# Performance work log

Hardware: AMD Instinct MI355X
Metric: run time of the kernel (lower is better)

Reference implementation:

```python
import jax, jax.numpy as jnp
import numpy as np

E, S, L, H, C = 32, 64, 20, 512, 32  # episodes, steps, max_comm_len, hidden_size, comm_shape
STD_MIN, STD_MAX = 2.0611536e-09, 7.389056  # exp(-20), exp(2)


def setup_inputs() -> dict:
    key = jax.random.key(0)
    ks = jax.random.split(key, 12)
    def p(k, shape):
        return jax.random.normal(k, shape, jnp.float32) * 0.02
    return {
        'x': jax.random.normal(ks[0], (E, S, H), jnp.float32),
        'Wr': p(ks[1], (2 * H, H)), 'br': jnp.zeros((H,), jnp.float32),
        'Wz': p(ks[2], (2 * H, H)), 'bz': jnp.zeros((H,), jnp.float32),
        'Wn': p(ks[3], (2 * H, H)), 'bn': jnp.zeros((H,), jnp.float32),
        'conv_w1': p(ks[4], (H // 4, H, 1)), 'conv_b1': jnp.zeros((H // 4,), jnp.float32),
        'conv_w3': p(ks[5], (H // 4, H, 3)), 'conv_b3': jnp.zeros((H // 4,), jnp.float32),
        'conv_w5': p(ks[6], (H // 4, H, 5)), 'conv_b5': jnp.zeros((H // 4,), jnp.float32),
        'conv_w7': p(ks[7], (H // 4, H, 7)), 'conv_b7': jnp.zeros((H // 4,), jnp.float32),
        'prelu_a': jnp.asarray(0.25, jnp.float32),
        'W_mu': p(ks[8], (H, C)), 'b_mu': jnp.zeros((C,), jnp.float32),
        'W_std': p(ks[9], (H, C)), 'b_std': jnp.zeros((C,), jnp.float32),
        'eps': jax.random.normal(ks[10], (E, S, L, C), jnp.float32),
    }


def reference(x, Wr, br, Wz, bz, Wn, bn,
              conv_w1, conv_b1, conv_w3, conv_b3, conv_w5, conv_b5, conv_w7, conv_b7,
              prelu_a, W_mu, b_mu, W_std, b_std, eps):
    B = E * S
    xf = x.reshape(B, H)  # same input fed to the RNN at every comm step

    def step(h, _):
        xh = jnp.concatenate([xf, h], -1)
        r = jax.nn.sigmoid(xh @ Wr + br)
        z = jax.nn.sigmoid(xh @ Wz + bz)
        n = jnp.tanh(jnp.concatenate([xf, r * h], -1) @ Wn + bn)
        h_new = (1.0 - z) * n + z * h  # time_constant=1 -> h = new GRU state
        return h_new, h_new

    h0 = jnp.zeros((B, H), x.dtype)
    _, hs = jax.lax.scan(step, h0, None, length=L)  # (L, B, H)
    comm_h = jnp.transpose(hs, (1, 2, 0))  # (B, H, L) -- NCW layout for conv

    dn = ('NCH', 'OIH', 'NCH')
    def conv(w, b, k):
        pad = (k - 1) // 2
        y = jax.lax.conv_general_dilated(comm_h, w, (1,), [(pad, pad)], dimension_numbers=dn)
        return y + b[None, :, None]

    y = jnp.concatenate([
        conv(conv_w1, conv_b1, 1),
        conv(conv_w3, conv_b3, 3),
        conv(conv_w5, conv_b5, 5),
        conv(conv_w7, conv_b7, 7),
    ], axis=1)  # (B, H, L)
    y = jnp.where(y >= 0, y, prelu_a * y)  # PReLU; dropout is identity in eval
    y = jnp.transpose(y, (0, 2, 1)).reshape(E, S, L, H)

    mu = y @ W_mu + b_mu
    std = jnp.clip(jax.nn.softplus(y @ W_std + b_std), STD_MIN, STD_MAX)
    comm = mu + eps * std  # reparameterized Normal sample
    comm_out = jnp.tanh(comm)
    log2pi = jnp.asarray(np.log(2.0 * np.pi), jnp.float32)
    log_prob = (-0.5 * ((comm - mu) / std) ** 2 - jnp.log(std) - 0.5 * log2pi
                - jnp.log(1.0 - comm_out ** 2 + 1e-6))
    log_prob = jnp.mean(log_prob, -1, keepdims=True)  # (E,S,L,1)
    log_prob = jnp.mean(log_prob, -2)  # (E,S,1)
    return comm_out, log_prob
```

## Files before the change

kernel.cpp:

```cpp
#include <hip/hip_runtime.h>
#include <hip/hip_bf16.h>

typedef __hip_bfloat16 bf16;
typedef short short8 __attribute__((ext_vector_type(8)));
typedef float floatx4 __attribute__((ext_vector_type(4)));

#define BDIM 2048
#define HDIM 512
#define LDIM 20
#define CDIM 32

__device__ __forceinline__ float sigm(float x) { return 1.0f / (1.0f + expf(-x)); }

__device__ __forceinline__ void ll16(const short* g, short* l)
{
    __builtin_amdgcn_global_load_lds(
        (const __attribute__((address_space(1))) void*)g,
        (__attribute__((address_space(3))) void*)l, 16, 0, 0);
}
#define WAITVM(N) asm volatile("s_waitcnt vmcnt(" #N ")" ::: "memory")

__device__ __forceinline__ void gemm_tile_ll(
    const short* __restrict__ A, int lda,
    const short* __restrict__ Bt, int ldb,
    int K, short* lds, floatx4 (&acc)[4][4], int tid)
{
    short* As = lds;
    short* Bs = lds + 128 * 32;
    const int wave = tid >> 6, lane = tid & 63;
    const int wm = wave & 1, wn = wave >> 1;
    const int m16 = lane & 15, quad = lane >> 4;
    const int lrow = lane >> 2;
    const int lcol = (lane & 3) * 8;

    for (int k0 = 0; k0 < K; k0 += 32) {
        __syncthreads();
#pragma unroll
        for (int seg = 0; seg < 2; ++seg) {
            const int sg = wave + seg * 4;
            ll16(A  + (size_t)(sg * 16 + lrow) * lda + k0 + lcol, As + sg * 512);
            ll16(Bt + (size_t)(sg * 16 + lrow) * ldb + k0 + lcol, Bs + sg * 512);
        }
        WAITVM(0);
        __syncthreads();
        short8 af[4], bfr[4];
#pragma unroll
        for (int i = 0; i < 4; ++i)
            af[i] = *(short8*)(As + (wm * 64 + i * 16 + m16) * 32 + quad * 8);
#pragma unroll
        for (int j = 0; j < 4; ++j)
            bfr[j] = *(short8*)(Bs + (wn * 64 + j * 16 + m16) * 32 + quad * 8);
#pragma unroll
        for (int i = 0; i < 4; ++i)
#pragma unroll
            for (int j = 0; j < 4; ++j)
                acc[i][j] = __builtin_amdgcn_mfma_f32_16x16x32_bf16(
                    af[i], bfr[j], acc[i][j], 0, 0, 0);
    }
}

__global__ __launch_bounds__(256) void k_prep_all(
    const float* __restrict__ x, bf16* __restrict__ xb,
    const float* __restrict__ Wr, const float* __restrict__ Wz,
    const float* __restrict__ Wn, bf16* __restrict__ Wfrag,
    const float* __restrict__ w1, const float* __restrict__ w3,
    const float* __restrict__ w5, const float* __restrict__ w7,
    bf16* __restrict__ wt,
    const float* __restrict__ Wmu, const float* __restrict__ Wstd,
    bf16* __restrict__ Wh_t, bf16* __restrict__ Wx_t,
    unsigned* __restrict__ ctr)
{
    __shared__ float tile[32][33];
    const int bid = blockIdx.x, tid = threadIdx.x;
    if (bid < 4096) {
        int i = bid * 256 + tid;
        xb[i] = (bf16)x[i];
    } else if (bid < 7168) {
        int idx = (bid - 4096) * 256 + tid;
        int e = idx & 7, lane = (idx >> 3) & 63;
        int t2 = idx >> 9;
        int f = t2 % 6, jk = t2 / 6;
        int kc = jk & 15, j = jk >> 4;
        int ftype = f >> 1;
        int col = j * 32 + (f & 1) * 16 + (lane & 15);
        int k = kc * 32 + ((lane >> 4) << 3) + e;
        const float* W = (ftype == 0) ? Wr : (ftype == 1) ? Wz : Wn;
        Wfrag[idx] = (bf16)W[(size_t)(512 + k) * 512 + col];
    } else if (bid < 11264) {
        int idx = (bid - 7168) * 256 + tid;
        int g, base;
        if (idx < 65536)       { g = 0; base = 0;      }
        else if (idx < 262144) { g = 1; base = 65536;  }
        else if (idx < 589824) { g = 2; base = 262144; }
        else                   { g = 3; base = 589824; }
        int rel = idx - base;
        int k = 2 * g + 1;
        int ci = rel & 511;
        int t2 = rel >> 9;
        int co = t2 & 127;
        int tap = t2 >> 7;
        const float* w = (g == 0) ? w1 : (g == 1) ? w3 : (g == 2) ? w5 : w7;
        wt[idx] = (bf16)w[((size_t)co * 512 + ci) * k + tap];
    } else if (bid < 11392) {
        int idx = (bid - 11264) * 256 + tid;
        int n = idx >> 9, k = idx & 511;
        float v = (n < 32) ? Wmu[(size_t)k * 32 + n]
                           : Wstd[(size_t)k * 32 + (n - 32)];
        Wh_t[idx] = (bf16)v;
    } else if (bid < 12160) {
        int rel = bid - 11392;
        int z = rel >> 8, xy = rel & 255;
        const float* src = (z == 0) ? Wr : (z == 1) ? Wz : Wn;
        bf16* d = Wx_t + (size_t)z * 262144;
        int tx = tid & 31, ty = tid >> 5;
        int k0 = (xy & 15) * 32, n0 = (xy >> 4) * 32;
#pragma unroll
        for (int i = 0; i < 32; i += 8)
            tile[ty + i][tx] = src[(size_t)(k0 + ty + i) * 512 + n0 + tx];
        __syncthreads();
#pragma unroll
        for (int i = 0; i < 32; i += 8)
            d[(size_t)(n0 + ty + i) * 512 + k0 + tx] = (bf16)tile[tx][ty + i];
    } else {
        ((unsigned*)ctr)[tid * 2]     = 0u;
        ((unsigned*)ctr)[tid * 2 + 1] = 0u;
    }
}

__global__ __launch_bounds__(256) void k_gx(
    const bf16* __restrict__ xb, const bf16* __restrict__ Wx_t,
    const float* __restrict__ br, const float* __restrict__ bz,
    const float* __restrict__ bn, bf16* __restrict__ gxb)
{
    __shared__ short lds[2 * 128 * 32];
    const int tid = threadIdx.x;
    const int row0 = blockIdx.x * 128, col0 = blockIdx.y * 128;
    floatx4 acc[4][4];
#pragma unroll
    for (int i = 0; i < 4; ++i)
#pragma unroll
        for (int j = 0; j < 4; ++j) acc[i][j] = (floatx4)0.0f;
    gemm_tile_ll((const short*)xb + (size_t)row0 * 512, 512,
                 (const short*)Wx_t + (size_t)col0 * 512, 512, 512, lds, acc, tid);
    const int wave = tid >> 6, lane = tid & 63;
    const int wm = wave & 1, wn = wave >> 1;
    const int m16 = lane & 15, quad = lane >> 4;
#pragma unroll
    for (int i = 0; i < 4; ++i)
#pragma unroll
        for (int j = 0; j < 4; ++j)
#pragma unroll
            for (int reg = 0; reg < 4; ++reg) {
                int b = row0 + wm * 64 + i * 16 + quad * 4 + reg;
                int n = col0 + wn * 64 + j * 16 + m16;
                float bias = (n < 512) ? br[n] : (n < 1024) ? bz[n - 512] : bn[n - 1024];
                gxb[(size_t)b * 1536 + n] = (bf16)(acc[i][j][reg] + bias);
            }
}

__device__ __forceinline__ void gbar2(unsigned* flags, int j, unsigned target,
                                      bool fast, int tid)
{
    WAITVM(0);
    __syncthreads();
    if (tid < 64) {
        if (tid == 0) {
            if (!fast) __threadfence();
            __hip_atomic_store(flags + j, target, __ATOMIC_RELAXED,
                               __HIP_MEMORY_SCOPE_AGENT);
        }
        unsigned v; int guard = 0;
        do {
            v = (tid < 16) ? __hip_atomic_load(flags + tid, __ATOMIC_RELAXED,
                                               __HIP_MEMORY_SCOPE_AGENT)
                           : target;
        } while (__ballot(v >= target) != ~0ull && ++guard < (1 << 18));
        if (!fast) { if (tid == 0) __threadfence(); }
        else asm volatile("buffer_inv" ::: "memory");
    }
    __syncthreads();
}

template<int NF>
__device__ __forceinline__ void phase_reg(
    const short* __restrict__ srcw, const short* __restrict__ wl,
    int f0, int lane, floatx4 (&acc)[NF])
{
    const short* g = srcw + (size_t)(lane & 15) * 512 + (lane >> 4) * 8;
    short8 a[16];
#pragma unroll
    for (int kc = 0; kc < 16; ++kc)
        a[kc] = *(const short8*)(g + kc * 32);
#pragma unroll
    for (int kc = 0; kc < 16; ++kc) {
        short8 bfr[NF];
#pragma unroll
        for (int f = 0; f < NF; ++f)
            bfr[f] = *(short8*)(wl + ((kc * 6 + f0 + f) << 9) + lane * 8);
#pragma unroll
        for (int f = 0; f < NF; ++f)
            acc[f] = __builtin_amdgcn_mfma_f32_16x16x32_bf16(a[kc], bfr[f],
                                                             acc[f], 0, 0, 0);
    }
}

__global__ __launch_bounds__(512, 2) void k_gru9(
    const bf16* __restrict__ Wfrag, const bf16* __restrict__ gxb,
    bf16* __restrict__ hs, bf16* __restrict__ rhb,
    unsigned* __restrict__ ctr, int* __restrict__ xcdtab)
{
    __shared__ short wlds[6 * 16 * 512];
    const int tid = threadIdx.x;
    const int wave = tid >> 6, lane = tid & 63;
    const int m16 = lane & 15, quad = lane >> 4;
    const int b = blockIdx.x;
    const int s = b >> 3;
    const int m = (b & 7) + ((s & 1) << 3);
    const int j = s >> 1;
    const int wrow = wave * 16;
    unsigned* flg  = ctr + m * 32;
    unsigned* vflg = ctr + m * 32 + 16;

    int myxcd;
    asm volatile("s_getreg_b32 %0, hwreg(HW_REG_XCC_ID)" : "=s"(myxcd));
    myxcd &= 15;
    if (tid == 0) xcdtab[m * 16 + j] = myxcd;

    const short* wsrc = (const short*)Wfrag + (size_t)j * 49152;
#pragma unroll
    for (int r = 0; r < 12; ++r)
        ll16(wsrc + ((wave * 12 + r) << 9) + lane * 8, wlds + ((wave * 12 + r) << 9));

    float gxr[2][4], gxz[2][4], gxn[2][4];
#pragma unroll
    for (int reg = 0; reg < 4; ++reg) {
        const bf16* gp = gxb + (size_t)(m * 128 + wrow + quad * 4 + reg) * 1536 + j * 32;
#pragma unroll
        for (int fc = 0; fc < 2; ++fc) {
            int c = fc * 16 + m16;
            gxr[fc][reg] = __bfloat162float(gp[c]);
            gxz[fc][reg] = __bfloat162float(gp[512 + c]);
            gxn[fc][reg] = __bfloat162float(gp[1024 + c]);
        }
    }

    gbar2(vflg, j, 1u, false, tid);
    bool fast = true;
#pragma unroll
    for (int jj = 0; jj < 16; ++jj) {
        int xv = __hip_atomic_load((const int*)xcdtab + m * 16 + jj,
                                   __ATOMIC_RELAXED, __HIP_MEMORY_SCOPE_AGENT);
        fast = fast && (xv == myxcd);
    }

    float h32[2][4];
    float zf[2][4];
    unsigned nbar = 0;
    const int rowg = m * 128 + wrow + quad * 4;

#pragma unroll
    for (int fc = 0; fc < 2; ++fc)
#pragma unroll
        for (int reg = 0; reg < 4; ++reg) {
            float z = sigm(gxz[fc][reg]);
            float nv = tanhf(gxn[fc][reg]);
            float hn = (1.0f - z) * nv;
            h32[fc][reg] = hn;
            hs[(size_t)(rowg + reg) * 512 + j * 32 + fc * 16 + m16] = (bf16)hn;
        }
    ++nbar; gbar2(flg, j, nbar, fast, tid);

    for (int t = 1; t < LDIM; ++t) {
        floatx4 acc[4];
#pragma unroll
        for (int f = 0; f < 4; ++f) acc[f] = (floatx4)0.0f;
        phase_reg<4>((const short*)hs + ((size_t)(t - 1) * BDIM + m * 128 + wrow) * 512,
                     wlds, 0, lane, acc);
#pragma unroll
        for (int fc = 0; fc < 2; ++fc)
#pragma unroll
            for (int reg = 0; reg < 4; ++reg) {
                float r = sigm(acc[fc][reg] + gxr[fc][reg]);
                zf[fc][reg] = sigm(acc[2 + fc][reg] + gxz[fc][reg]);
                rhb[(size_t)(rowg + reg) * 512 + j * 32 + fc * 16 + m16] =
                    (bf16)(r * h32[fc][reg]);
            }
        ++nbar; gbar2(flg, j, nbar, fast, tid);
        floatx4 acc2[2];
#pragma unroll
        for (int f = 0; f < 2; ++f) acc2[f] = (floatx4)0.0f;
        phase_reg<2>((const short*)rhb + (size_t)(m * 128 + wrow) * 512,
                     wlds, 4, lane, acc2);
#pragma unroll
        for (int fc = 0; fc < 2; ++fc)
#pragma unroll
            for (int reg = 0; reg < 4; ++reg) {
                float nv = tanhf(acc2[fc][reg] + gxn[fc][reg]);
                float z = zf[fc][reg];
                float hn = (1.0f - z) * nv + z * h32[fc][reg];
                h32[fc][reg] = hn;
                hs[((size_t)t * BDIM + rowg + reg) * 512 + j * 32 + fc * 16 + m16] =
                    (bf16)hn;
            }
        if (t < LDIM - 1) { ++nbar; gbar2(flg, j, nbar, fast, tid); }
    }
}

__global__ __launch_bounds__(256) void k_conv(
    const bf16* __restrict__ hs, const bf16* __restrict__ Wc_t,
    const float* __restrict__ b1, const float* __restrict__ b3,
    const float* __restrict__ b5, const float* __restrict__ b7,
    const float* __restrict__ pa, bf16* __restrict__ y)
{
    __shared__ short lds[2 * 128 * 32];
    const int tid = threadIdx.x;
    const int bid = blockIdx.x;
    const int xcd = bid & 7;
    const int idx = bid >> 3;
    const int half = idx / 80;
    const int btile = xcd + 8 * half;
    const int gl = idx % 80;
    const int g = 3 - (gl / 20);
    const int l = gl % 20;
    const int row0 = btile * 128;
    const int ktap = 2 * g + 1, p = g;
    const int offs[4] = {0, 65536, 262144, 589824};
    const short* Wg = (const short*)Wc_t + offs[g];
    floatx4 acc[4][4];
#pragma unroll
    for (int i = 0; i < 4; ++i)
#pragma unroll
        for (int j = 0; j < 4; ++j) acc[i][j] = (floatx4)0.0f;
    for (int tap = 0; tap < ktap; ++tap) {
        int li = l + tap - p;
        if (li < 0 || li >= LDIM) continue;
        gemm_tile_ll((const short*)hs + (size_t)li * BDIM * HDIM + (size_t)row0 * 512, 512,
                     Wg + (size_t)tap * 128 * 512, 512, 512, lds, acc, tid);
    }
    const float* bp = (g == 0) ? b1 : (g == 1) ? b3 : (g == 2) ? b5 : b7;
    const float a = *pa;
    const int wave = tid >> 6, lane = tid & 63;
    const int wm = wave & 1, wn = wave >> 1;
    const int m16 = lane & 15, quad = lane >> 4;
#pragma unroll
    for (int i = 0; i < 4; ++i)
#pragma unroll
        for (int j = 0; j < 4; ++j)
#pragma unroll
            for (int reg = 0; reg < 4; ++reg) {
                int b = row0 + wm * 64 + i * 16 + quad * 4 + reg;
                int col = wn * 64 + j * 16 + m16;
                float v = acc[i][j][reg] + bp[col];
                v = (v >= 0.0f) ? v : a * v;
                y[((size_t)b * LDIM + l) * 512 + g * 128 + col] = (bf16)v;
            }
}

__global__ __launch_bounds__(256) void k_head2(
    const bf16* __restrict__ y, const bf16* __restrict__ Wh_t,
    const float* __restrict__ bmu, const float* __restrict__ bstd,
    const float* __restrict__ eps, float* __restrict__ out_comm,
    float* __restrict__ lpsum)
{
    __shared__ short As[128 * 32];
    __shared__ short Bs[64 * 32];
    const int tid = threadIdx.x;
    const int wave = tid >> 6, lane = tid & 63;
    const int m16 = lane & 15, quad = lane >> 4;
    const int lrow = lane >> 2, lcol = (lane & 3) * 8;
    const int row0 = blockIdx.x * 128;
    floatx4 acc[2][4];
#pragma unroll
    for (int i = 0; i < 2; ++i)
#pragma unroll
        for (int j = 0; j < 4; ++j) acc[i][j] = (floatx4)0.0f;
    const short* Ap = (const short*)y + (size_t)row0 * 512;
    const short* Bp = (const short*)Wh_t;
    for (int k0 = 0; k0 < 512; k0 += 32) {
        __syncthreads();
        ll16(Ap + (size_t)(wave * 16 + lrow) * 512 + k0 + lcol, As + wave * 512);
        ll16(Ap + (size_t)((wave + 4) * 16 + lrow) * 512 + k0 + lcol,
             As + (wave + 4) * 512);
        ll16(Bp + (size_t)(wave * 16 + lrow) * 512 + k0 + lcol, Bs + wave * 512);
        WAITVM(0);
        __syncthreads();
        short8 af[2], bfr[4];
#pragma unroll
        for (int i = 0; i < 2; ++i)
            af[i] = *(short8*)(As + (wave * 32 + i * 16 + m16) * 32 + quad * 8);
#pragma unroll
        for (int j = 0; j < 4; ++j)
            bfr[j] = *(short8*)(Bs + (j * 16 + m16) * 32 + quad * 8);
#pragma unroll
        for (int i = 0; i < 2; ++i)
#pragma unroll
            for (int j = 0; j < 4; ++j)
                acc[i][j] = __builtin_amdgcn_mfma_f32_16x16x32_bf16(
                    af[i], bfr[j], acc[i][j], 0, 0, 0);
    }
#pragma unroll
    for (int i = 0; i < 2; ++i)
#pragma unroll
        for (int reg = 0; reg < 4; ++reg) {
            int row = row0 + wave * 32 + i * 16 + quad * 4 + reg;
            float lp = 0.0f;
#pragma unroll
            for (int jj = 0; jj < 2; ++jj) {
                int c = jj * 16 + m16;
                float mu = acc[i][jj][reg] + bmu[c];
                float sraw = acc[i][jj + 2][reg] + bstd[c];
                float sp = (sraw > 20.0f) ? sraw : log1pf(expf(sraw));
                float sd = fminf(fmaxf(sp, 2.0611536e-09f), 7.389056f);
                float e = eps[(size_t)row * 32 + c];
                float comm = fmaf(e, sd, mu);
                float tt = tanhf(comm);
                out_comm[(size_t)row * 32 + c] = tt;
                lp += -0.5f * e * e - logf(sd) - 0.91893853320467274f
                      - logf(1.0f - tt * tt + 1e-6f);
            }
            lp += __shfl_xor(lp, 1, 16);
            lp += __shfl_xor(lp, 2, 16);
            lp += __shfl_xor(lp, 4, 16);
            lp += __shfl_xor(lp, 8, 16);
            if (m16 == 0) lpsum[row] = lp;
        }
}

__global__ __launch_bounds__(256) void k_final(const float* __restrict__ lpsum,
                                               float* __restrict__ out2)
{
    int b = blockIdx.x * 256 + threadIdx.x;
    if (b < BDIM) {
        float s = 0.0f;
#pragma unroll
        for (int i = 0; i < LDIM; ++i) s += lpsum[b * LDIM + i];
        out2[b] = s * (1.0f / (LDIM * CDIM));
    }
}

extern "C" void kernel_launch(void* const* d_in, const int* in_sizes, int n_in,
                              void* d_out, int out_size, void* d_ws, size_t ws_size,
                              hipStream_t stream)
{
    const float* x    = (const float*)d_in[0];
    const float* Wr   = (const float*)d_in[1];
    const float* br   = (const float*)d_in[2];
    const float* Wz   = (const float*)d_in[3];
    const float* bz   = (const float*)d_in[4];
    const float* Wn   = (const float*)d_in[5];
    const float* bn   = (const float*)d_in[6];
    const float* w1   = (const float*)d_in[7];
    const float* b1   = (const float*)d_in[8];
    const float* w3   = (const float*)d_in[9];
    const float* b3   = (const float*)d_in[10];
    const float* w5   = (const float*)d_in[11];
    const float* b5   = (const float*)d_in[12];
    const float* w7   = (const float*)d_in[13];
    const float* b7   = (const float*)d_in[14];
    const float* pa   = (const float*)d_in[15];
    const float* Wmu  = (const float*)d_in[16];
    const float* bmu  = (const float*)d_in[17];
    const float* Wstd = (const float*)d_in[18];
    const float* bstd = (const float*)d_in[19];
    const float* eps  = (const float*)d_in[20];

    char* cur = (char*)d_ws;
    auto alloc = [&](size_t bytes) -> void* {
        void* r = (void*)cur;
        cur += (bytes + 255) & ~(size_t)255;
        return r;
    };
    const size_t BH = (size_t)BDIM * HDIM;
    bf16*  gxb   = (bf16*)alloc((size_t)BDIM * 1536 * 2);
    bf16*  xb    = (bf16*)alloc(BH * 2);
    bf16*  hs    = (bf16*)alloc(BH * LDIM * 2);
    bf16*  ybuf  = (bf16*)alloc(BH * LDIM * 2);
    bf16*  Wx_t  = (bf16*)alloc((size_t)1536 * 512 * 2);
    bf16*  Wfrag = (bf16*)alloc((size_t)786432 * 2);
    bf16*  Wc_t  = (bf16*)alloc((size_t)1048576 * 2);
    bf16*  Wh_t  = (bf16*)alloc((size_t)64 * 512 * 2);
    bf16*  rhb   = (bf16*)alloc((size_t)BDIM * 512 * 2);
    float* lpsum = (float*)alloc((size_t)BDIM * LDIM * 4);
    unsigned* ctr = (unsigned*)alloc(2048);
    int*   xcdtab = (int*)alloc(1024);

    k_prep_all<<<12161, 256, 0, stream>>>(x, xb, Wr, Wz, Wn, Wfrag,
                                          w1, w3, w5, w7, Wc_t, Wmu, Wstd,
                                          Wh_t, Wx_t, ctr);

    k_gx<<<dim3(16, 12), 256, 0, stream>>>(xb, Wx_t, br, bz, bn, gxb);

    k_gru9<<<256, 512, 0, stream>>>(Wfrag, gxb, hs, rhb, ctr, xcdtab);

    k_conv<<<1280, 256, 0, stream>>>(hs, Wc_t, b1, b3, b5, b7, pa, ybuf);

    float* out_comm = (float*)d_out;
    float* out_lp   = (float*)d_out + (size_t)BDIM * LDIM * CDIM;
    k_head2<<<320, 256, 0, stream>>>(ybuf, Wh_t, bmu, bstd, eps, out_comm, lpsum);
    k_final<<<8, 256, 0, stream>>>(lpsum, out_lp);
}
```

Baseline: 474.0 us.

## Fuse input-gate GEMM into GRU kernel and fold final log-prob reduction into head

Measured after the change: 475.9 us. Within noise of the previous version (+0.4%).

```diff
diff --git a/kernel.cpp b/kernel.cpp
--- a/kernel.cpp
+++ b/kernel.cpp
@@ -67,10 +67,9 @@
     const float* __restrict__ w5, const float* __restrict__ w7,
     bf16* __restrict__ wt,
     const float* __restrict__ Wmu, const float* __restrict__ Wstd,
-    bf16* __restrict__ Wh_t, bf16* __restrict__ Wx_t,
-    unsigned* __restrict__ ctr)
-{
-    __shared__ float tile[32][33];
+    bf16* __restrict__ Wh_t, bf16* __restrict__ WxF,
+    float* __restrict__ out_lp, unsigned* __restrict__ ctr)
+{
     const int bid = blockIdx.x, tid = threadIdx.x;
     if (bid < 4096) {
         int i = bid * 256 + tid;
@@ -107,55 +106,23 @@
         float v = (n < 32) ? Wmu[(size_t)k * 32 + n]
                            : Wstd[(size_t)k * 32 + (n - 32)];
         Wh_t[idx] = (bf16)v;
-    } else if (bid < 12160) {
-        int rel = bid - 11392;
-        int z = rel >> 8, xy = rel & 255;
-        const float* src = (z == 0) ? Wr : (z == 1) ? Wz : Wn;
-        bf16* d = Wx_t + (size_t)z * 262144;
-        int tx = tid & 31, ty = tid >> 5;
-        int k0 = (xy & 15) * 32, n0 = (xy >> 4) * 32;
-#pragma unroll
-        for (int i = 0; i < 32; i += 8)
-            tile[ty + i][tx] = src[(size_t)(k0 + ty + i) * 512 + n0 + tx];
-        __syncthreads();
-#pragma unroll
-        for (int i = 0; i < 32; i += 8)
-            d[(size_t)(n0 + ty + i) * 512 + k0 + tx] = (bf16)tile[tx][ty + i];
+    } else if (bid < 14464) {
+        int idx = (bid - 11392) * 256 + tid;
+        int e = idx & 7, lane = (idx >> 3) & 63;
+        int t2 = idx >> 9;
+        int f = t2 % 6, jk = t2 / 6;
+        int kc = jk & 15, j = jk >> 4;
+        int ftype = f >> 1;
+        int col = j * 32 + (f & 1) * 16 + (lane & 15);
+        int k = kc * 32 + ((lane >> 4) << 3) + e;
+        const float* W = (ftype == 0) ? Wr : (ftype == 1) ? Wz : Wn;
+        WxF[idx] = (bf16)W[(size_t)k * 512 + col];
+    } else if (bid < 14472) {
+        out_lp[(bid - 14464) * 256 + tid] = 0.0f;
     } else {
-        ((unsigned*)ctr)[tid * 2]     = 0u;
-        ((unsigned*)ctr)[tid * 2 + 1] = 0u;
-    }
-}
-
-__global__ __launch_bounds__(256) void k_gx(
-    const bf16* __restrict__ xb, const bf16* __restrict__ Wx_t,
-    const float* __restrict__ br, const float* __restrict__ bz,
-    const float* __restrict__ bn, bf16* __restrict__ gxb)
-{
-    __shared__ short lds[2 * 128 * 32];
-    const int tid = threadIdx.x;
-    const int row0 = blockIdx.x * 128, col0 = blockIdx.y * 128;
-    floatx4 acc[4][4];
-#pragma unroll
-    for (int i = 0; i < 4; ++i)
-#pragma unroll
-        for (int j = 0; j < 4; ++j) acc[i][j] = (floatx4)0.0f;
-    gemm_tile_ll((const short*)xb + (size_t)row0 * 512, 512,
-                 (const short*)Wx_t + (size_t)col0 * 512, 512, 512, lds, acc, tid);
-    const int wave = tid >> 6, lane = tid & 63;
-    const int wm = wave & 1, wn = wave >> 1;
-    const int m16 = lane & 15, quad = lane >> 4;
-#pragma unroll
-    for (int i = 0; i < 4; ++i)
-#pragma unroll
-        for (int j = 0; j < 4; ++j)
-#pragma unroll
-            for (int reg = 0; reg < 4; ++reg) {
-                int b = row0 + wm * 64 + i * 16 + quad * 4 + reg;
-                int n = col0 + wn * 64 + j * 16 + m16;
-                float bias = (n < 512) ? br[n] : (n < 1024) ? bz[n - 512] : bn[n - 1024];
-                gxb[(size_t)b * 1536 + n] = (bf16)(acc[i][j][reg] + bias);
-            }
+        ctr[tid * 2]     = 0u;
+        ctr[tid * 2 + 1] = 0u;
+    }
 }
 
 __device__ __forceinline__ void gbar2(unsigned* flags, int j, unsigned target,
@@ -204,8 +171,11 @@
     }
 }
 
-__global__ __launch_bounds__(512, 2) void k_gru9(
-    const bf16* __restrict__ Wfrag, const bf16* __restrict__ gxb,
+__global__ __launch_bounds__(512, 2) void k_gru15(
+    const bf16* __restrict__ Wfrag, const bf16* __restrict__ WxF,
+    const bf16* __restrict__ xb,
+    const float* __restrict__ br, const float* __restrict__ bz,
+    const float* __restrict__ bn,
     bf16* __restrict__ hs, bf16* __restrict__ rhb,
     unsigned* __restrict__ ctr, int* __restrict__ xcdtab)
 {
@@ -226,6 +196,27 @@
     myxcd &= 15;
     if (tid == 0) xcdtab[m * 16 + j] = myxcd;
 
+    floatx4 ga[6];
+#pragma unroll
+    for (int f = 0; f < 6; ++f) ga[f] = (floatx4)0.0f;
+    {
+        const short* xg = (const short*)xb +
+            (size_t)(m * 128 + wrow + m16) * 512 + quad * 8;
+        const short* wxg = (const short*)WxF + (size_t)j * 49152 + lane * 8;
+#pragma unroll
+        for (int kc = 0; kc < 16; ++kc) {
+            short8 a = *(const short8*)(xg + kc * 32);
+            short8 bfr[6];
+#pragma unroll
+            for (int f = 0; f < 6; ++f)
+                bfr[f] = *(const short8*)(wxg + ((kc * 6 + f) << 9));
+#pragma unroll
+            for (int f = 0; f < 6; ++f)
+                ga[f] = __builtin_amdgcn_mfma_f32_16x16x32_bf16(a, bfr[f],
+                                                                ga[f], 0, 0, 0);
+        }
+    }
+
     const short* wsrc = (const short*)Wfrag + (size_t)j * 49152;
 #pragma unroll
     for (int r = 0; r < 12; ++r)
@@ -233,14 +224,14 @@
 
     float gxr[2][4], gxz[2][4], gxn[2][4];
 #pragma unroll
-    for (int reg = 0; reg < 4; ++reg) {
-        const bf16* gp = gxb + (size_t)(m * 128 + wrow + quad * 4 + reg) * 1536 + j * 32;
-#pragma unroll
-        for (int fc = 0; fc < 2; ++fc) {
-            int c = fc * 16 + m16;
-            gxr[fc][reg] = __bfloat162float(gp[c]);
-            gxz[fc][reg] = __bfloat162float(gp[512 + c]);
-            gxn[fc][reg] = __bfloat162float(gp[1024 + c]);
+    for (int fc = 0; fc < 2; ++fc) {
+        int col = j * 32 + fc * 16 + m16;
+        float vbr = br[col], vbz = bz[col], vbn = bn[col];
+#pragma unroll
+        for (int reg = 0; reg < 4; ++reg) {
+            gxr[fc][reg] = ga[fc][reg] + vbr;
+            gxz[fc][reg] = ga[2 + fc][reg] + vbz;
+            gxn[fc][reg] = ga[4 + fc][reg] + vbn;
         }
     }
 
@@ -360,7 +351,7 @@
     const bf16* __restrict__ y, const bf16* __restrict__ Wh_t,
     const float* __restrict__ bmu, const float* __restrict__ bstd,
     const float* __restrict__ eps, float* __restrict__ out_comm,
-    float* __restrict__ lpsum)
+    float* __restrict__ out_lp)
 {
     __shared__ short As[128 * 32];
     __shared__ short Bs[64 * 32];
@@ -422,20 +413,9 @@
             lp += __shfl_xor(lp, 2, 16);
             lp += __shfl_xor(lp, 4, 16);
             lp += __shfl_xor(lp, 8, 16);
-            if (m16 == 0) lpsum[row] = lp;
-        }
-}
-
-__global__ __launch_bounds__(256) void k_final(const float* __restrict__ lpsum,
-                                               float* __restrict__ out2)
-{
-    int b = blockIdx.x * 256 + threadIdx.x;
-    if (b < BDIM) {
-        float s = 0.0f;
-#pragma unroll
-        for (int i = 0; i < LDIM; ++i) s += lpsum[b * LDIM + i];
-        out2[b] = s * (1.0f / (LDIM * CDIM));
-    }
+            if (m16 == 0)
+                atomicAdd(out_lp + row / LDIM, lp * (1.0f / (LDIM * CDIM)));
+        }
 }
 
 extern "C" void kernel_launch(void* const* d_in, const int* in_sizes, int n_in,
@@ -471,31 +451,29 @@
         return r;
     };
     const size_t BH = (size_t)BDIM * HDIM;
-    bf16*  gxb   = (bf16*)alloc((size_t)BDIM * 1536 * 2);
     bf16*  xb    = (bf16*)alloc(BH * 2);
     bf16*  hs    = (bf16*)alloc(BH * LDIM * 2);
     bf16*  ybuf  = (bf16*)alloc(BH * LDIM * 2);
-    bf16*  Wx_t  = (bf16*)alloc((size_t)1536 * 512 * 2);
     bf16*  Wfrag = (bf16*)alloc((size_t)786432 * 2);
+    bf16*  WxF   = (bf16*)alloc((size_t)786432 * 2);
     bf16*  Wc_t  = (bf16*)alloc((size_t)1048576 * 2);
     bf16*  Wh_t  = (bf16*)alloc((size_t)64 * 512 * 2);
     bf16*  rhb   = (bf16*)alloc((size_t)BDIM * 512 * 2);
-    float* lpsum = (float*)alloc((size_t)BDIM * LDIM * 4);
     unsigned* ctr = (unsigned*)alloc(2048);
     int*   xcdtab = (int*)alloc(1024);
 
-    k_prep_all<<<12161, 256, 0, stream>>>(x, xb, Wr, Wz, Wn, Wfrag,
-                                          w1, w3, w5, w7, Wc_t, Wmu, Wstd,
-                                          Wh_t, Wx_t, ctr);
-
-    k_gx<<<dim3(16, 12), 256, 0, stream>>>(xb, Wx_t, br, bz, bn, gxb);
-
-    k_gru9<<<256, 512, 0, stream>>>(Wfrag, gxb, hs, rhb, ctr, xcdtab);
-
-    k_conv<<<1280, 256, 0, stream>>>(hs, Wc_t, b1, b3, b5, b7, pa, ybuf);
-
     float* out_comm = (float*)d_out;
     float* out_lp   = (float*)d_out + (size_t)BDIM * LDIM * CDIM;
-    k_head2<<<320, 256, 0, stream>>>(ybuf, Wh_t, bmu, bstd, eps, out_comm, lpsum);
-    k_final<<<8, 256, 0, stream>>>(lpsum, out_lp);
-}
+
+    k_prep_all<<<14473, 256, 0, stream>>>(x, xb, Wr, Wz, Wn, Wfrag,
+                                          w1, w3, w5, w7, Wc_t, Wmu, Wstd,
+                                          Wh_t, WxF, out_lp, ctr);
+
+    k_gru15<<<256, 512, 0, stream>>>(Wfrag, WxF, xb, br, bz, bn,
+                                     hs, rhb, ctr, xcdtab);
+
+    k_conv<<<1280, 256, 0, stream>>>(hs, Wc_t, b1, b3, b5, b7, pa, ybuf);
+
+    k_head2<<<320, 256, 0, stream>>>(ybuf, Wh_t, bmu, bstd, eps,
+                                     out_comm, out_lp);
+}
```
